# Kernel optimization log

Hardware: AMD Instinct MI355X
Metric: run time of the kernel (lower is better)

The kernel has to match this reference:

```python
import jax, jax.numpy as jnp
import numpy as np

NEG_INF = -1e9
LRELU_SLOPE = 0.2  # torch GAT default leaky_relu negative slope


def setup_inputs() -> dict:
    key = jax.random.key(0)
    k1, k2, k3, k4, k5 = jax.random.split(key, 5)
    N, F_IN, H, DH = 4096, 1433, 8, 8  # n_nodes, in_features, n_heads, per-head dim (n_hidden=64)
    vert = jax.random.normal(k1, (N, F_IN), dtype=jnp.float32)
    edge = jax.random.randint(k2, (N, N), 0, 2, dtype=jnp.int32)  # dense adjacency mask
    W = jax.random.normal(k3, (F_IN, H * DH), dtype=jnp.float32) * 0.05
    a_l = jax.random.normal(k4, (H, DH), dtype=jnp.float32) * 0.05
    a_r = jax.random.normal(k5, (H, DH), dtype=jnp.float32) * 0.05
    return {"vert": vert, "edge": edge, "W": W, "a_l": a_l, "a_r": a_r}


def reference(vert, edge, W, a_l, a_r):
    # GAT-style edge-affinity layer (is_concat=True) + ELU; dropout is identity (eval mode).
    N = vert.shape[0]
    H, DH = a_l.shape
    g = (vert @ W).reshape(N, H, DH)                      # [N,H,Dh] projected node features
    sl = jnp.einsum('nhd,hd->nh', g, a_l)                 # source-node attention term
    sr = jnp.einsum('nhd,hd->nh', g, a_r)                 # target-node attention term
    e = sl[:, None, :] + sr[None, :, :]                   # [N,N,H]: attn([g_i || g_j])
    e = jnp.where(e >= 0, e, LRELU_SLOPE * e)             # leaky_relu
    mask = (edge != 0)[:, :, None]                        # [N,N,1]
    e = jnp.where(mask, e, NEG_INF)                       # mask non-edges
    a = jax.nn.softmax(e, axis=1)                         # normalize over neighbors j
    out = jnp.einsum('ijh,jhd->ihd', a, g).reshape(N, H * DH)  # aggregate + concat heads
    return jax.nn.elu(out)
```

## Files before the change

kernel.cpp:

```cpp
#include <hip/hip_runtime.h>
#include <hip/hip_bf16.h>

#define NN 4096
#define FIN 1433
#define NH 8
#define DH 8
#define HD 64
#define KP 1472
#define LOG2E 1.44269504f
#define NJS 8
#define ITB 32
#define NCHK ((NN / NJS) / 64)
#define NKS 4

typedef unsigned int u32;
typedef unsigned long long u64;
typedef float v4f __attribute__((ext_vector_type(4)));
typedef _Float16 f16;
typedef _Float16 h2 __attribute__((ext_vector_type(2)));
typedef _Float16 f16x8 __attribute__((ext_vector_type(8)));

static __device__ __forceinline__ short f2h16(float f) {
    union { f16 h; short s; } u; u.h = (f16)f; return u.s;
}
static __device__ __forceinline__ h2 u2h2(u32 x) {
    union { u32 u; h2 h; } v; v.u = x; return v.h;
}
static __device__ __forceinline__ u32 h22u(h2 x) {
    union { h2 h; u32 u; } v; v.h = x; return v.u;
}

#if __has_builtin(__builtin_amdgcn_sbfe)
#define SBFE1(x, k) __builtin_amdgcn_sbfe((int)(x), (k), 1)
#else
#define SBFE1(x, k) (((int)((x) << (31 - (k)))) >> 31)
#endif

static __device__ __forceinline__ void gload_lds16(const void* g, void* l) {
    __builtin_amdgcn_global_load_lds(
        (const __attribute__((address_space(1))) void*)g,
        (__attribute__((address_space(3))) void*)l, 16, 0, 0);
}

__global__ __launch_bounds__(256) void k_eprep(const int* __restrict__ edge,
                                               uint4* __restrict__ emask) {
    const int t = threadIdx.x, lane = t & 63, w = t >> 6;
    const int row = blockIdx.x;
    const int* erow = edge + (size_t)row * NN;
    uint4* mrow = emask + (size_t)row * (NN / 128);
#pragma unroll
    for (int it = 0; it < 8; ++it) {
        const int ck = w * 8 + it;
        const int2 e2 = *(const int2*)&erow[ck * 128 + 2 * lane];
        const u64 bA = __ballot(e2.x != 0);
        const u64 bB = __ballot(e2.y != 0);
        if (lane == 0)
            mrow[ck] = (uint4){(u32)bA, (u32)bB, (u32)(bA >> 32), (u32)(bB >> 32)};
    }
}

__global__ __launch_bounds__(256) void k_wprep(const float* __restrict__ W,
                                               short* __restrict__ Wt) {
    __shared__ float Ts[64][65];
    const int c = blockIdx.x;
    const int u = threadIdx.x;
    const int n4 = (u & 15) * 4;
    const int kr = u >> 4;
#pragma unroll
    for (int q = 0; q < 4; ++q) {
        const int kl = kr + q * 16;
        const int kg = c * 64 + kl;
        v4f v = {0.f, 0.f, 0.f, 0.f};
        if (kg < FIN) v = *(const v4f*)&W[(size_t)kg * HD + n4];
        *(v4f*)&Ts[kl][n4] = v;
    }
    __syncthreads();
    const int n = u >> 2;
    const int koff = (u & 3) * 16;
    __align__(16) short tmp[16];
#pragma unroll
    for (int r = 0; r < 16; ++r) tmp[r] = f2h16(Ts[koff + r][n]);
    *(uint4*)&Wt[(size_t)n * KP + c * 64 + koff]     = *(uint4*)&tmp[0];
    *(uint4*)&Wt[(size_t)n * KP + c * 64 + koff + 8] = *(uint4*)&tmp[8];
}

__global__ __launch_bounds__(256, 4) void k_gemm(
    const float* __restrict__ vert, const short* __restrict__ Wt,
    float* __restrict__ Cp)
{
    __shared__ float cacc[4][16][68];

    const int t = threadIdx.x, lane = t & 63, w = t >> 6;
    const int ml = lane & 15, q = lane >> 4;
    const int i0 = blockIdx.x * 16;
    const int ks = blockIdx.y;
    const float* vrow = vert + (size_t)(i0 + ml) * FIN;

    v4f acc[4];
#pragma unroll
    for (int g = 0; g < 4; ++g) acc[g] = (v4f){0.f, 0.f, 0.f, 0.f};

    for (int c = ks + 4 * w; c < 45; c += 16) {
        const int k0 = c * 32 + q * 8;
        v4f a0, a1;
        if (k0 + 7 < FIN) {
            a0 = *(const v4f*)&vrow[k0];
            a1 = *(const v4f*)&vrow[k0 + 4];
        } else {
            float tmp[8];
#pragma unroll
            for (int e = 0; e < 8; ++e)
                tmp[e] = (k0 + e < FIN) ? vrow[k0 + e] : 0.f;
            a0 = (v4f){tmp[0], tmp[1], tmp[2], tmp[3]};
            a1 = (v4f){tmp[4], tmp[5], tmp[6], tmp[7]};
        }
        const f16x8 af = {(f16)a0.x, (f16)a0.y, (f16)a0.z, (f16)a0.w,
                          (f16)a1.x, (f16)a1.y, (f16)a1.z, (f16)a1.w};
#pragma unroll
        for (int g = 0; g < 4; ++g) {
            const f16x8 bf = *(const f16x8*)&Wt[(size_t)(g * 16 + ml) * KP + k0];
            acc[g] = __builtin_amdgcn_mfma_f32_16x16x32_f16(af, bf, acc[g], 0, 0, 0);
        }
    }

#pragma unroll
    for (int g = 0; g < 4; ++g)
#pragma unroll
        for (int r = 0; r < 4; ++r)
            cacc[w][q * 4 + r][g * 16 + ml] = acc[g][r];
    __syncthreads();

    const int m = t >> 4, n4 = (t & 15) * 4;
    v4f s = (v4f){0.f, 0.f, 0.f, 0.f};
#pragma unroll
    for (int ww = 0; ww < 4; ++ww) s += *(const v4f*)&cacc[ww][m][n4];
    *(v4f*)&Cp[((size_t)ks * NN + i0 + m) * HD + n4] = s;
}

__global__ __launch_bounds__(256) void k_gpost(
    const float* __restrict__ Cp,
    const float* __restrict__ al, const float* __restrict__ ar,
    short* __restrict__ gT, short* __restrict__ eB, short* __restrict__ eD,
    float* __restrict__ Rw)
{
    const int t = threadIdx.x;
    const int gid = blockIdx.x * 256 + t;
    const int i = gid >> 4, n4 = (gid & 15) * 4;

    v4f s = (v4f){0.f, 0.f, 0.f, 0.f};
#pragma unroll
    for (int ks = 0; ks < NKS; ++ks)
        s += *(const v4f*)&Cp[((size_t)ks * NN + i) * HD + n4];

#pragma unroll
    for (int e = 0; e < 4; ++e)
        gT[(size_t)(n4 + e) * NN + i] = f2h16(s[e]);

    float pl = s.x * al[n4] + s.y * al[n4 + 1] + s.z * al[n4 + 2] + s.w * al[n4 + 3];
    float pr = s.x * ar[n4] + s.y * ar[n4 + 1] + s.z * ar[n4 + 2] + s.w * ar[n4 + 3];
    pl += __shfl_xor(pl, 1, 64);
    pr += __shfl_xor(pr, 1, 64);
    if ((t & 1) == 0) {
        const int h = (t & 15) >> 1;
        eB[h * NN + i] = f2h16(exp2f(pr * LOG2E));
        eD[h * NN + i] = f2h16(exp2f(0.2f * pr * LOG2E));
        Rw[i * NH + h] = exp2f(-0.8f * pl * LOG2E);
    }
}

__global__ __launch_bounds__(256, 4) void k_attn(
    const uint4* __restrict__ emask, const short* __restrict__ gT,
    const short* __restrict__ eB, const short* __restrict__ eD,
    const float* __restrict__ Rw,
    float* __restrict__ numw, float* __restrict__ denw)
{
    __shared__ __align__(16) short Gs[2][64 * 64];
    __shared__ __align__(16) short BDs[2][8 * 128];

    const int t = threadIdx.x, lane = t & 63, w = t >> 6;
    const int ml = lane & 15, quad = lane >> 4;
    const int m8 = ml & 7;
    const int i0 = blockIdx.x * ITB;
    const int js = blockIdx.y;
    const int jbase = js * (NN / NJS);
    const int h0 = w, h1 = w + 4;
    const int qb4 = quad * 4;
    const bool mhi = (ml >= 8);
    const u32 one2 = 0x3C003C00u;
    const uint4 ones4 = (uint4){one2, one2, one2, one2};

    h2 Ri[2][2];
#pragma unroll
    for (int sub = 0; sub < 2; ++sub) {
        const f16 r0 = (f16)Rw[(i0 + sub * 16 + ml) * NH + h0];
        const f16 r1 = (f16)Rw[(i0 + sub * 16 + ml) * NH + h1];
        Ri[sub][0] = (h2){r0, r0};
        Ri[sub][1] = (h2){r1, r1};
    }

    const uint2* mrow0 = (const uint2*)emask + (size_t)(i0 + ml) * (NN / 64) + js * NCHK;
    const uint2* mrow1 = (const uint2*)emask + (size_t)(i0 + 16 + ml) * (NN / 64) + js * NCHK;

    const short *gsrc0, *gsrc1;
    {
        int u = t, row = u >> 3;
        gsrc0 = gT + (size_t)row * NN + jbase + (((u & 7) * 8) ^ ((row & 7) * 8));
        u = 256 + t; row = u >> 3;
        gsrc1 = gT + (size_t)row * NN + jbase + (((u & 7) * 8) ^ ((row & 7) * 8));
    }
    const short* bdsrc = nullptr;
    if (t < 128) {
        const int head = t >> 4, slot = t & 15;
        bdsrc = (slot < 8 ? eB : eD) + (size_t)head * NN + jbase + (slot & 7) * 8;
    }
    const int wub = (t & ~63) * 16;

#define STAGE(buf, ck)                                                        \
    do {                                                                      \
        const int jc_ = (ck) * 64;                                            \
        gload_lds16(gsrc0 + jc_, (char*)Gs[buf] + wub);                       \
        gload_lds16(gsrc1 + jc_, (char*)Gs[buf] + 4096 + wub);                \
        if (t < 128) gload_lds16(bdsrc + jc_, (char*)BDs[buf] + wub);         \
    } while (0)

    v4f acc[2][2];
#pragma unroll
    for (int sub = 0; sub < 2; ++sub) {
        acc[sub][0] = (v4f){0.f, 0.f, 0.f, 0.f};
        acc[sub][1] = (v4f){0.f, 0.f, 0.f, 0.f};
    }

    STAGE(0, 0);
    uint2 mw0 = mrow0[0], mw1 = mrow1[0], pm0, pm1;

    for (int c = 0; c < NCHK; ++c) {
        const int cb = c & 1, nb = cb ^ 1;
        __syncthreads();
        const bool pf = (c + 1) < NCHK;
        if (pf) {
            STAGE(nb, c + 1);
            pm0 = mrow0[c + 1];
            pm1 = mrow1[c + 1];
        }
#pragma unroll
        for (int s = 0; s < 2; ++s) {
            const int xj = s * 32 + quad * 8;
            const int xg = xj ^ (m8 * 8);
            union { uint4 u; f16x8 h; } g0u, g1u;
            g0u.u = mhi ? ones4 : *(const uint4*)&Gs[cb][(h0 * 8 + m8) * 64 + xg];
            g1u.u = mhi ? ones4 : *(const uint4*)&Gs[cb][(h1 * 8 + m8) * 64 + xg];
            const uint4 bu0 = *(const uint4*)&BDs[cb][h0 * 128 + xj];
            const uint4 du0 = *(const uint4*)&BDs[cb][h0 * 128 + 64 + xj];
            const uint4 bu1 = *(const uint4*)&BDs[cb][h1 * 128 + xj];
            const uint4 du1 = *(const uint4*)&BDs[cb][h1 * 128 + 64 + xj];
            const int base = (s << 4) + qb4;
#pragma unroll
            for (int sub = 0; sub < 2; ++sub) {
                const u32 WA = (sub ? mw1.x : mw0.x) >> base;
                const u32 WB = (sub ? mw1.y : mw0.y) >> base;
                u32 m[4];
#pragma unroll
                for (int k = 0; k < 4; ++k) {
                    const int ea = SBFE1(WA, k);
                    const int eb = SBFE1(WB, k);
                    m[k] = __builtin_amdgcn_perm((u32)eb, (u32)ea, 0x05040100u);
                }
                u32 aw0[4], aw1[4];
#pragma unroll
                for (int k = 0; k < 4; ++k) {
                    const u32 rd0 = h22u(Ri[sub][0] * u2h2((&du0.x)[k]));
                    const u32 rd1 = h22u(Ri[sub][1] * u2h2((&du1.x)[k]));
                    u32 p0, p1;
                    asm("v_pk_max_f16 %0, %1, %2" : "=v"(p0) : "v"(rd0), "v"((&bu0.x)[k]));
                    asm("v_pk_max_f16 %0, %1, %2" : "=v"(p1) : "v"(rd1), "v"((&bu1.x)[k]));
                    aw0[k] = p0 & m[k];
                    aw1[k] = p1 & m[k];
                }
                union { uint4 u; f16x8 h; } a0u, a1u;
                a0u.u = (uint4){aw0[0], aw0[1], aw0[2], aw0[3]};
                a1u.u = (uint4){aw1[0], aw1[1], aw1[2], aw1[3]};
                acc[sub][0] = __builtin_amdgcn_mfma_f32_16x16x32_f16(
                    a0u.h, g0u.h, acc[sub][0], 0, 0, 0);
                acc[sub][1] = __builtin_amdgcn_mfma_f32_16x16x32_f16(
                    a1u.h, g1u.h, acc[sub][1], 0, 0, 0);
            }
        }
        if (pf) { mw0 = pm0; mw1 = pm1; }
    }
#undef STAGE

    float* nw = numw + (size_t)js * NN * HD;
    float* dw = denw + (size_t)js * NN * NH;
#pragma unroll
    for (int sub = 0; sub < 2; ++sub) {
        const int ibase = i0 + sub * 16 + quad * 4;
#pragma unroll
        for (int hh = 0; hh < 2; ++hh) {
            const int h = w + hh * 4;
#pragma unroll
            for (int r = 0; r < 4; ++r) {
                if (ml < 8)       nw[(ibase + r) * HD + h * 8 + ml] = acc[sub][hh][r];
                else if (ml == 8) dw[(ibase + r) * NH + h]          = acc[sub][hh][r];
            }
        }
    }
}

__global__ __launch_bounds__(256) void k_comb(
    const float* __restrict__ numw, const float* __restrict__ denw,
    float* __restrict__ out)
{
    const int gid = blockIdx.x * 256 + threadIdx.x;
    const int i = gid >> 6, h = (gid & 63) >> 3;
    float num = 0.f, den = 0.f;
#pragma unroll
    for (int s = 0; s < NJS; ++s) {
        num += numw[(size_t)s * NN * HD + gid];
        den += denw[(size_t)s * NN * NH + i * NH + h];
    }
    float x = num / den;
    out[gid] = (x > 0.f) ? x : (__expf(x) - 1.f);
}

extern "C" void kernel_launch(void* const* d_in, const int* in_sizes, int n_in,
                              void* d_out, int out_size, void* d_ws, size_t ws_size,
                              hipStream_t stream) {
    const float* vert = (const float*)d_in[0];
    const int*   edge = (const int*)d_in[1];
    const float* W    = (const float*)d_in[2];
    const float* al   = (const float*)d_in[3];
    const float* ar   = (const float*)d_in[4];
    float* out = (float*)d_out;

    char* ws = (char*)d_ws;
    short* gT    = (short*)ws;
    short* eB    = (short*)(ws + 512 * 1024);
    short* eD    = (short*)(ws + 576 * 1024);
    float* Rw    = (float*)(ws + 640 * 1024);
    short* Wt    = (short*)(ws + 768 * 1024);
    uint4* emask = (uint4*)(ws + 1024 * 1024);
    float* Cp    = (float*)(ws + 3 * 1024 * 1024);
    float* numw  = (float*)(ws + 7 * 1024 * 1024);
    float* denw  = (float*)(ws + 15 * 1024 * 1024);

    hipLaunchKernelGGL(k_eprep, dim3(NN), dim3(256), 0, stream, edge, emask);
    hipLaunchKernelGGL(k_wprep, dim3(23), dim3(256), 0, stream, W, Wt);
    hipLaunchKernelGGL(k_gemm, dim3(NN / 16, NKS), dim3(256), 0, stream,
                       vert, Wt, Cp);
    hipLaunchKernelGGL(k_gpost, dim3(NN * 16 / 256), dim3(256), 0, stream,
                       Cp, al, ar, gT, eB, eD, Rw);
    hipLaunchKernelGGL(k_attn, dim3(NN / ITB, NJS), dim3(256), 0, stream,
                       emask, gT, eB, eD, Rw, numw, denw);
    hipLaunchKernelGGL(k_comb, dim3(NN * HD / 256), dim3(256), 0, stream,
                       numw, denw, out);
}
```

Before: 154.8 us.

## Fuse edge-mask bit packing into attention kernel via per-chunk ballots

Removes the separate k_eprep pass that packed the int32 adjacency matrix into bitmasks. The attention kernel now streams edge rows directly with nontemporal loads, ballots them into 64-bit masks in shared memory, and double-buffers them alongside the gT/eB/eD staging. This drops one kernel launch and the write and reread of the packed mask buffer. In exchange, the attention kernel takes on the 64MB edge read, which adds register pressure and latency inside its main loop, and the bit order of the mask words changes to match the new layout.

```diff
diff --git a/kernel.cpp b/kernel.cpp
--- a/kernel.cpp
+++ b/kernel.cpp
@@ -42,23 +42,6 @@
         (__attribute__((address_space(3))) void*)l, 16, 0, 0);
 }
 
-__global__ __launch_bounds__(256) void k_eprep(const int* __restrict__ edge,
-                                               uint4* __restrict__ emask) {
-    const int t = threadIdx.x, lane = t & 63, w = t >> 6;
-    const int row = blockIdx.x;
-    const int* erow = edge + (size_t)row * NN;
-    uint4* mrow = emask + (size_t)row * (NN / 128);
-#pragma unroll
-    for (int it = 0; it < 8; ++it) {
-        const int ck = w * 8 + it;
-        const int2 e2 = *(const int2*)&erow[ck * 128 + 2 * lane];
-        const u64 bA = __ballot(e2.x != 0);
-        const u64 bB = __ballot(e2.y != 0);
-        if (lane == 0)
-            mrow[ck] = (uint4){(u32)bA, (u32)bB, (u32)(bA >> 32), (u32)(bB >> 32)};
-    }
-}
-
 __global__ __launch_bounds__(256) void k_wprep(const float* __restrict__ W,
                                                short* __restrict__ Wt) {
     __shared__ float Ts[64][65];
@@ -169,13 +152,14 @@
 }
 
 __global__ __launch_bounds__(256, 4) void k_attn(
-    const uint4* __restrict__ emask, const short* __restrict__ gT,
+    const int* __restrict__ edge, const short* __restrict__ gT,
     const short* __restrict__ eB, const short* __restrict__ eD,
     const float* __restrict__ Rw,
     float* __restrict__ numw, float* __restrict__ denw)
 {
     __shared__ __align__(16) short Gs[2][64 * 64];
     __shared__ __align__(16) short BDs[2][8 * 128];
+    __shared__ __align__(16) u64 Ms[2][ITB];
 
     const int t = threadIdx.x, lane = t & 63, w = t >> 6;
     const int ml = lane & 15, quad = lane >> 4;
@@ -184,7 +168,6 @@
     const int js = blockIdx.y;
     const int jbase = js * (NN / NJS);
     const int h0 = w, h1 = w + 4;
-    const int qb4 = quad * 4;
     const bool mhi = (ml >= 8);
     const u32 one2 = 0x3C003C00u;
     const uint4 ones4 = (uint4){one2, one2, one2, one2};
@@ -197,9 +180,6 @@
         Ri[sub][0] = (h2){r0, r0};
         Ri[sub][1] = (h2){r1, r1};
     }
-
-    const uint2* mrow0 = (const uint2*)emask + (size_t)(i0 + ml) * (NN / 64) + js * NCHK;
-    const uint2* mrow1 = (const uint2*)emask + (size_t)(i0 + 16 + ml) * (NN / 64) + js * NCHK;
 
     const short *gsrc0, *gsrc1;
     {
@@ -214,6 +194,9 @@
         bdsrc = (slot < 8 ? eB : eD) + (size_t)head * NN + jbase + (slot & 7) * 8;
     }
     const int wub = (t & ~63) * 16;
+
+    const int* ebase = edge + (size_t)(i0 + w * 8) * NN + jbase + lane;
+    u32 er[8];
 
 #define STAGE(buf, ck)                                                        \
     do {                                                                      \
@@ -223,6 +206,23 @@
         if (t < 128) gload_lds16(bdsrc + jc_, (char*)BDs[buf] + wub);         \
     } while (0)
 
+#define ELOAD(ck)                                                             \
+    do {                                                                      \
+        const int jo_ = (ck) * 64;                                            \
+        _Pragma("unroll")                                                     \
+        for (int rr = 0; rr < 8; ++rr)                                        \
+            er[rr] = __builtin_nontemporal_load(ebase + (size_t)rr * NN + jo_); \
+    } while (0)
+
+#define EBALLOT(buf)                                                          \
+    do {                                                                      \
+        _Pragma("unroll")                                                     \
+        for (int rr = 0; rr < 8; ++rr) {                                      \
+            const u64 b_ = __ballot(er[rr] != 0);                             \
+            if (lane == 0) Ms[buf][w * 8 + rr] = b_;                          \
+        }                                                                     \
+    } while (0)
+
     v4f acc[2][2];
 #pragma unroll
     for (int sub = 0; sub < 2; ++sub) {
@@ -231,17 +231,19 @@
     }
 
     STAGE(0, 0);
-    uint2 mw0 = mrow0[0], mw1 = mrow1[0], pm0, pm1;
+    ELOAD(0);
+    EBALLOT(0);
 
     for (int c = 0; c < NCHK; ++c) {
         const int cb = c & 1, nb = cb ^ 1;
         __syncthreads();
         const bool pf = (c + 1) < NCHK;
-        if (pf) {
-            STAGE(nb, c + 1);
-            pm0 = mrow0[c + 1];
-            pm1 = mrow1[c + 1];
-        }
+        if (pf) { STAGE(nb, c + 1); ELOAD(c + 1); }
+
+        union { u64 q; uint2 d; } m0u, m1u;
+        m0u.q = Ms[cb][ml];
+        m1u.q = Ms[cb][16 + ml];
+
 #pragma unroll
         for (int s = 0; s < 2; ++s) {
             const int xj = s * 32 + quad * 8;
@@ -253,16 +255,16 @@
             const uint4 du0 = *(const uint4*)&BDs[cb][h0 * 128 + 64 + xj];
             const uint4 bu1 = *(const uint4*)&BDs[cb][h1 * 128 + xj];
             const uint4 du1 = *(const uint4*)&BDs[cb][h1 * 128 + 64 + xj];
-            const int base = (s << 4) + qb4;
 #pragma unroll
             for (int sub = 0; sub < 2; ++sub) {
-                const u32 WA = (sub ? mw1.x : mw0.x) >> base;
-                const u32 WB = (sub ? mw1.y : mw0.y) >> base;
+                const u32 half = sub ? ((s ? m1u.d.y : m1u.d.x))
+                                     : ((s ? m0u.d.y : m0u.d.x));
+                const u32 w8 = half >> (quad * 8);
                 u32 m[4];
 #pragma unroll
                 for (int k = 0; k < 4; ++k) {
-                    const int ea = SBFE1(WA, k);
-                    const int eb = SBFE1(WB, k);
+                    const int ea = SBFE1(w8, 2 * k);
+                    const int eb = SBFE1(w8, 2 * k + 1);
                     m[k] = __builtin_amdgcn_perm((u32)eb, (u32)ea, 0x05040100u);
                 }
                 u32 aw0[4], aw1[4];
@@ -285,9 +287,11 @@
                     a1u.h, g1u.h, acc[sub][1], 0, 0, 0);
             }
         }
-        if (pf) { mw0 = pm0; mw1 = pm1; }
+        if (pf) EBALLOT(nb);
     }
 #undef STAGE
+#undef ELOAD
+#undef EBALLOT
 
     float* nw = numw + (size_t)js * NN * HD;
     float* dw = denw + (size_t)js * NN * NH;
@@ -338,19 +342,17 @@
     short* eD    = (short*)(ws + 576 * 1024);
     float* Rw    = (float*)(ws + 640 * 1024);
     short* Wt    = (short*)(ws + 768 * 1024);
-    uint4* emask = (uint4*)(ws + 1024 * 1024);
     float* Cp    = (float*)(ws + 3 * 1024 * 1024);
     float* numw  = (float*)(ws + 7 * 1024 * 1024);
     float* denw  = (float*)(ws + 15 * 1024 * 1024);
 
-    hipLaunchKernelGGL(k_eprep, dim3(NN), dim3(256), 0, stream, edge, emask);
     hipLaunchKernelGGL(k_wprep, dim3(23), dim3(256), 0, stream, W, Wt);
     hipLaunchKernelGGL(k_gemm, dim3(NN / 16, NKS), dim3(256), 0, stream,
                        vert, Wt, Cp);
     hipLaunchKernelGGL(k_gpost, dim3(NN * 16 / 256), dim3(256), 0, stream,
                        Cp, al, ar, gT, eB, eD, Rw);
     hipLaunchKernelGGL(k_attn, dim3(NN / ITB, NJS), dim3(256), 0, stream,
-                       emask, gT, eB, eD, Rw, numw, denw);
+                       edge, gT, eB, eD, Rw, numw, denw);
     hipLaunchKernelGGL(k_comb, dim3(NN * HD / 256), dim3(256), 0, stream,
                        numw, denw, out);
 }
```

Result: faster. 150.1 us, median of 2 (-3.0%).
